# Performance work log

Hardware: AMD Instinct MI355X
Metric: run time of the kernel (lower is better)

Reference implementation:

```python
import jax, jax.numpy as jnp
import numpy as np

TS = 6      # texture cube size (hard-coded in module)
S = 256     # image size (NMR default / ref image size)
DIST = 2.732


def _look_at(verts, eye):
    # NMR look_at: camera at eye, looking at origin, up=(0,1,0)
    eye = jnp.asarray(eye, verts.dtype)
    z = -eye / jnp.linalg.norm(eye)
    up = jnp.array([0.0, 1.0, 0.0], verts.dtype)
    x = jnp.cross(up, z)
    x = x / jnp.linalg.norm(x)
    y = jnp.cross(z, x)
    R = jnp.stack([x, y, z])          # rows = camera axes
    return (verts - eye) @ R.T


def _render(verts, faces, tex_flat, eye):
    # verts [V,3], faces [F,3] int, tex_flat [F*TS^3, 3] (tanh already applied)
    v = _look_at(verts, eye)
    fv = v[faces]                      # [F,3,3]
    p0, p1, p2 = fv[:, 0], fv[:, 1], fv[:, 2]
    ps = (2.0 * jnp.arange(S, dtype=verts.dtype) + 1.0 - S) / S
    PX = jnp.broadcast_to(ps[None, :], (S, S)).reshape(-1)      # x right
    PY = jnp.broadcast_to(-ps[:, None], (S, S)).reshape(-1)     # y up (row 0 = top)

    def edge(a, b):
        # signed edge function, [F,HW]
        return ((PX[None, :] - a[:, 0:1]) * (b[:, 1:2] - a[:, 1:2])
                - (PY[None, :] - a[:, 1:2]) * (b[:, 0:1] - a[:, 0:1]))

    e0 = edge(p1, p2)
    e1 = edge(p2, p0)
    e2 = edge(p0, p1)
    # per-face signed area (double area) [F,1]
    area = ((p1[:, 0] - p0[:, 0]) * (p2[:, 1] - p0[:, 1])
            - (p1[:, 1] - p0[:, 1]) * (p2[:, 0] - p0[:, 0]))[:, None]
    ok = jnp.abs(area) > 1e-8
    inv = jnp.where(ok, 1.0 / jnp.where(ok, area, 1.0), 0.0)
    w0, w1, w2 = e0 * inv, e1 * inv, e2 * inv            # barycentric weights
    inside = (w0 >= 0) & (w1 >= 0) & (w2 >= 0) & ok       # both windings (fill_back)
    z = w0 * p0[:, 2:3] + w1 * p1[:, 2:3] + w2 * p2[:, 2:3]
    depth = jnp.where(inside & (z > 0), z, jnp.inf)       # z-buffer candidates
    best = jnp.argmin(depth, axis=0)                      # [HW] winning face
    hit = jnp.take_along_axis(depth, best[None, :], axis=0)[0] < jnp.inf
    wb = jnp.stack([jnp.take_along_axis(w, best[None, :], axis=0)[0]
                    for w in (w0, w1, w2)], axis=-1)       # [HW,3]
    ti = jnp.clip(jnp.round(wb * (TS - 1)), 0, TS - 1).astype(jnp.int32)
    flat = ((best * TS + ti[:, 0]) * TS + ti[:, 1]) * TS + ti[:, 2]
    colors = tex_flat[flat]                                # [HW,3] gather
    img = jnp.where(hit[:, None], colors, 0.0)
    return img.reshape(S, S, 3).transpose(2, 0, 1)[None]   # [1,3,S,S]


def setup_inputs() -> dict:
    key = jax.random.key(0)
    k1, k2, k3, k4, k5 = jax.random.split(key, 5)
    V, F = 252, 500
    return {
        "vertices": jax.random.normal(k1, (1, V, 3), jnp.float32),
        "faces": jax.random.randint(k2, (1, F, 3), 0, V, jnp.int64),
        "textures": jax.random.normal(k3, (1, F, TS, TS, TS, 3), jnp.float32),
        "image_ref": jax.random.uniform(k4, (1, 3, S, S), jnp.float32),
        "image_ref_2": jax.random.uniform(k5, (1, 3, S, S), jnp.float32),
    }


def reference(vertices, faces, textures, image_ref, image_ref_2):
    tex_flat = jnp.tanh(textures[0]).reshape(-1, 3)
    v, f = vertices[0], faces[0]
    # eye = get_points_from_angles(2.732, 180, 0) -> (0, 0, +d)
    img1 = _render(v, f, tex_flat, jnp.array([0.0, 0.0, DIST], jnp.float32))
    loss_one_side = jnp.sum((img1 - image_ref) ** 2)
    # eye = get_points_from_angles(2.732, 0, 0) -> (0, 0, -d)
    img2 = _render(v, f, tex_flat, jnp.array([0.0, 0.0, -DIST], jnp.float32))
    loss_symmetric = jnp.sum((img2 - image_ref_2) ** 2)
    return (loss_one_side + loss_symmetric) / 2
```

## Files before the change

kernel.cpp:

```cpp
#include <hip/hip_runtime.h>
#include <math.h>

#define IMG_S 256
#define NPIX (IMG_S * IMG_S)
#define NFACE 500
#define NCHUNK 16
#define FPC 32
#define PPT 8
#define TSZ 6
#define DIST 2.732f

struct FaceCoef {
    float A0, B0, C0, A1, B1, C1, A2, B2, C2, Az, Bz, Cz;
};

__device__ __forceinline__ void edge_coef(float ax, float ay, float bx, float by,
                                          float inv, float& A, float& B, float& C) {
    float dy = by - ay;
    float dx = bx - ax;
    A = dy * inv;
    B = -dx * inv;
    C = (ay * dx - ax * dy) * inv;
}

__device__ __forceinline__ FaceCoef compute_face(const float* __restrict__ verts,
                                                 const int* __restrict__ faces,
                                                 int f, int view) {
    int i0 = faces[f * 3 + 0];
    int i1 = faces[f * 3 + 1];
    int i2 = faces[f * 3 + 2];

    float v0x = verts[i0 * 3 + 0], v0y = verts[i0 * 3 + 1], v0z = verts[i0 * 3 + 2];
    float v1x = verts[i1 * 3 + 0], v1y = verts[i1 * 3 + 1], v1z = verts[i1 * 3 + 2];
    float v2x = verts[i2 * 3 + 0], v2y = verts[i2 * 3 + 1], v2z = verts[i2 * 3 + 2];

    float p0x, p0y, p0z, p1x, p1y, p1z, p2x, p2y, p2z;
    if (view == 0) {
        p0x = -v0x; p0y = v0y; p0z = DIST - v0z;
        p1x = -v1x; p1y = v1y; p1z = DIST - v1z;
        p2x = -v2x; p2y = v2y; p2z = DIST - v2z;
    } else {
        p0x = v0x; p0y = v0y; p0z = v0z + DIST;
        p1x = v1x; p1y = v1y; p1z = v1z + DIST;
        p2x = v2x; p2y = v2y; p2z = v2z + DIST;
    }

    float area = (p1x - p0x) * (p2y - p0y) - (p1y - p0y) * (p2x - p0x);
    bool ok = fabsf(area) > 1e-8f;

    FaceCoef fc;
    if (ok) {
        float inv = 1.0f / area;
        edge_coef(p1x, p1y, p2x, p2y, inv, fc.A0, fc.B0, fc.C0);
        edge_coef(p2x, p2y, p0x, p0y, inv, fc.A1, fc.B1, fc.C1);
        edge_coef(p0x, p0y, p1x, p1y, inv, fc.A2, fc.B2, fc.C2);
        fc.Az = fc.A0 * p0z + fc.A1 * p1z + fc.A2 * p2z;
        fc.Bz = fc.B0 * p0z + fc.B1 * p1z + fc.B2 * p2z;
        fc.Cz = fc.C0 * p0z + fc.C1 * p1z + fc.C2 * p2z;
    } else {
        fc.A0 = fc.B0 = fc.A1 = fc.B1 = fc.A2 = fc.B2 = 0.0f;
        fc.C0 = fc.C1 = fc.C2 = -1.0f;
        fc.Az = fc.Bz = fc.Cz = 0.0f;
    }
    return fc;
}

__device__ __forceinline__ float pix_x(int ix) {
    return (2.0f * (float)ix + 1.0f - (float)IMG_S) * (1.0f / (float)IMG_S);
}
__device__ __forceinline__ float pix_y(int iy) {
    return -((2.0f * (float)iy + 1.0f - (float)IMG_S) * (1.0f / (float)IMG_S));
}

__global__ __launch_bounds__(256) void raster_chunk_kernel(
    const float* __restrict__ verts,
    const int*   __restrict__ faces,
    unsigned long long* __restrict__ packed_out)
{
    __shared__ float4 fc[FPC][3];
    const int tile  = blockIdx.x;
    const int chunk = blockIdx.y;
    const int view  = blockIdx.z;
    const int fbase = chunk * FPC;

    if ((int)threadIdx.x < FPC) {
        int f = fbase + (int)threadIdx.x;
        FaceCoef c;
        if (f < NFACE) {
            c = compute_face(verts, faces, f, view);
        } else {
            c.A0 = c.B0 = c.A1 = c.B1 = c.A2 = c.B2 = 0.0f;
            c.C0 = c.C1 = c.C2 = -1.0f;
            c.Az = c.Bz = c.Cz = 0.0f;
        }
        fc[threadIdx.x][0] = make_float4(c.A0, c.B0, c.C0, c.A1);
        fc[threadIdx.x][1] = make_float4(c.B1, c.C1, c.A2, c.B2);
        fc[threadIdx.x][2] = make_float4(c.C2, c.Az, c.Bz, c.Cz);
    }
    __syncthreads();

    const int ix = threadIdx.x;
    const float px = pix_x(ix);
    float py[PPT];
    #pragma unroll
    for (int k = 0; k < PPT; ++k) py[k] = pix_y(tile * PPT + k);

    float bestz[PPT];
    int   besti[PPT];
    #pragma unroll
    for (int k = 0; k < PPT; ++k) { bestz[k] = INFINITY; besti[k] = -1; }

    float4 n0 = fc[0][0], n1 = fc[0][1], n2 = fc[0][2];
    #pragma unroll 4
    for (int f = 0; f < FPC; ++f) {
        float4 q0 = n0, q1 = n1, q2 = n2;
        int fn = (f + 1) & (FPC - 1);
        n0 = fc[fn][0]; n1 = fc[fn][1]; n2 = fc[fn][2];

        float d0 = fmaf(px, q0.x, q0.z);
        float d1 = fmaf(px, q0.w, q1.y);
        float d2 = fmaf(px, q1.z, q2.x);
        float dz = fmaf(px, q2.y, q2.w);
        #pragma unroll
        for (int k = 0; k < PPT; ++k) {
            float w0 = fmaf(q0.y, py[k], d0);
            float w1 = fmaf(q1.x, py[k], d1);
            float w2 = fmaf(q1.w, py[k], d2);
            float z  = fmaf(q2.z, py[k], dz);
            float wmin = fminf(w0, fminf(w1, w2));
            float s = fminf(z, bestz[k] - z);
            bool cc = (wmin >= 0.0f) && (s > 0.0f);
            bestz[k] = cc ? z : bestz[k];
            besti[k] = cc ? f : besti[k];
        }
    }

    unsigned long long* __restrict__ outp =
        packed_out + (size_t)(view * NCHUNK + chunk) * NPIX + tile * (PPT * IMG_S) + ix;
    #pragma unroll
    for (int k = 0; k < PPT; ++k) {
        unsigned long long packed;
        if (besti[k] >= 0)
            packed = ((unsigned long long)__float_as_uint(bestz[k]) << 32) |
                     (unsigned int)(fbase + besti[k]);
        else
            packed = ~0ull;
        outp[k * IMG_S] = packed;
    }
}

__global__ __launch_bounds__(256) void shade_loss_kernel(
    const float* __restrict__ verts,
    const int*   __restrict__ faces,
    const float* __restrict__ tex,
    const float* __restrict__ ref0,
    const float* __restrict__ ref1,
    const unsigned long long* __restrict__ packed_in,
    float* __restrict__ partials)
{
    __shared__ float red[4];
    const int gid  = blockIdx.x * blockDim.x + threadIdx.x;
    const int view = gid >> 16;
    const int pix  = gid & (NPIX - 1);

    const unsigned long long* p = packed_in + (size_t)view * NCHUNK * NPIX + pix;
    unsigned long long best = p[0];
    #pragma unroll
    for (int c = 1; c < NCHUNK; ++c) {
        unsigned long long v = p[(size_t)c * NPIX];
        best = (v < best) ? v : best;
    }

    float c0 = 0.0f, c1 = 0.0f, c2 = 0.0f;
    if (best != ~0ull) {
        int fidx = (int)(best & 0xFFFFFFFFu);
        FaceCoef fcw = compute_face(verts, faces, fidx, view);
        const float px = pix_x(pix & (IMG_S - 1));
        const float py = pix_y(pix >> 8);
        float w0 = fmaf(fcw.B0, py, fmaf(px, fcw.A0, fcw.C0));
        float w1 = fmaf(fcw.B1, py, fmaf(px, fcw.A1, fcw.C1));
        float w2 = fmaf(fcw.B2, py, fmaf(px, fcw.A2, fcw.C2));
        int t0 = (int)fminf(fmaxf(rintf(w0 * (float)(TSZ - 1)), 0.0f), (float)(TSZ - 1));
        int t1 = (int)fminf(fmaxf(rintf(w1 * (float)(TSZ - 1)), 0.0f), (float)(TSZ - 1));
        int t2 = (int)fminf(fmaxf(rintf(w2 * (float)(TSZ - 1)), 0.0f), (float)(TSZ - 1));
        int flat = ((fidx * TSZ + t0) * TSZ + t1) * TSZ + t2;
        const float* t = tex + (long)flat * 3;
        c0 = tanhf(t[0]);
        c1 = tanhf(t[1]);
        c2 = tanhf(t[2]);
    }

    const float* __restrict__ ref = (view == 0) ? ref0 : ref1;
    float d0 = c0 - ref[0 * NPIX + pix];
    float d1 = c1 - ref[1 * NPIX + pix];
    float d2 = c2 - ref[2 * NPIX + pix];
    float acc = fmaf(d0, d0, fmaf(d1, d1, d2 * d2));

    for (int off = 32; off > 0; off >>= 1)
        acc += __shfl_down(acc, off, 64);
    int lane = threadIdx.x & 63;
    int wid = threadIdx.x >> 6;
    if (lane == 0) red[wid] = acc;
    __syncthreads();
    if (threadIdx.x == 0)
        partials[blockIdx.x] = red[0] + red[1] + red[2] + red[3];
}

__global__ __launch_bounds__(256) void reduce_kernel(const float* __restrict__ partials,
                                                     int n, float* __restrict__ out) {
    __shared__ float red[4];
    float v = 0.0f;
    for (int i = threadIdx.x; i < n; i += 256) v += partials[i];
    for (int off = 32; off > 0; off >>= 1)
        v += __shfl_down(v, off, 64);
    int lane = threadIdx.x & 63;
    int wid = threadIdx.x >> 6;
    if (lane == 0) red[wid] = v;
    __syncthreads();
    if (threadIdx.x == 0)
        out[0] = 0.5f * (red[0] + red[1] + red[2] + red[3]);
}

extern "C" void kernel_launch(void* const* d_in, const int* in_sizes, int n_in,
                              void* d_out, int out_size, void* d_ws, size_t ws_size,
                              hipStream_t stream) {
    const float* verts = (const float*)d_in[0];
    const int*   faces = (const int*)d_in[1];
    const float* tex   = (const float*)d_in[2];
    const float* ref0  = (const float*)d_in[3];
    const float* ref1  = (const float*)d_in[4];
    float* out = (float*)d_out;

    unsigned long long* packed = (unsigned long long*)d_ws;
    float* partials = (float*)((char*)d_ws + (size_t)2 * NCHUNK * NPIX * 8);

    dim3 grid1(NPIX / (256 * PPT), NCHUNK, 2);
    raster_chunk_kernel<<<grid1, 256, 0, stream>>>(verts, faces, packed);

    const int shade_blocks = (2 * NPIX) / 256;
    shade_loss_kernel<<<shade_blocks, 256, 0, stream>>>(verts, faces, tex, ref0, ref1,
                                                        packed, partials);
    reduce_kernel<<<1, 256, 0, stream>>>(partials, shade_blocks, out);
}
```

Before: 90.76 us.

## Cull faces per row tile and merge chunk z-buffers with atomicMin

Each raster block now drops faces whose y-extent misses its 8-row tile, or that lie entirely behind the camera, and compacts the survivors with a ballot. The inner loop then iterates only over visible faces. Per-chunk results are merged straight into a single z-buffer per view with 64-bit atomicMin, so the shade kernel reads one value instead of 16 and the separate reduce kernel becomes a float atomicAdd. This cuts the 16x packed buffer traffic and the wasted edge tests. It adds two memsets, atomic contention and a non-deterministic float summation order.

```diff
diff --git a/kernel.cpp b/kernel.cpp
--- a/kernel.cpp
+++ b/kernel.cpp
@@ -23,9 +23,10 @@
     C = (ay * dx - ax * dy) * inv;
 }
 
-__device__ __forceinline__ FaceCoef compute_face(const float* __restrict__ verts,
-                                                 const int* __restrict__ faces,
-                                                 int f, int view) {
+__device__ __forceinline__ bool compute_face_bbox(const float* __restrict__ verts,
+                                                  const int* __restrict__ faces,
+                                                  int f, int view, FaceCoef& fc,
+                                                  float& ymin, float& ymax, float& zmax) {
     int i0 = faces[f * 3 + 0];
     int i1 = faces[f * 3 + 1];
     int i2 = faces[f * 3 + 2];
@@ -45,24 +46,22 @@
         p2x = v2x; p2y = v2y; p2z = v2z + DIST;
     }
 
+    ymin = fminf(p0y, fminf(p1y, p2y));
+    ymax = fmaxf(p0y, fmaxf(p1y, p2y));
+    zmax = fmaxf(p0z, fmaxf(p1z, p2z));
+
     float area = (p1x - p0x) * (p2y - p0y) - (p1y - p0y) * (p2x - p0x);
     bool ok = fabsf(area) > 1e-8f;
-
-    FaceCoef fc;
-    if (ok) {
-        float inv = 1.0f / area;
-        edge_coef(p1x, p1y, p2x, p2y, inv, fc.A0, fc.B0, fc.C0);
-        edge_coef(p2x, p2y, p0x, p0y, inv, fc.A1, fc.B1, fc.C1);
-        edge_coef(p0x, p0y, p1x, p1y, inv, fc.A2, fc.B2, fc.C2);
-        fc.Az = fc.A0 * p0z + fc.A1 * p1z + fc.A2 * p2z;
-        fc.Bz = fc.B0 * p0z + fc.B1 * p1z + fc.B2 * p2z;
-        fc.Cz = fc.C0 * p0z + fc.C1 * p1z + fc.C2 * p2z;
-    } else {
-        fc.A0 = fc.B0 = fc.A1 = fc.B1 = fc.A2 = fc.B2 = 0.0f;
-        fc.C0 = fc.C1 = fc.C2 = -1.0f;
-        fc.Az = fc.Bz = fc.Cz = 0.0f;
-    }
-    return fc;
+    if (!ok) return false;
+
+    float inv = 1.0f / area;
+    edge_coef(p1x, p1y, p2x, p2y, inv, fc.A0, fc.B0, fc.C0);
+    edge_coef(p2x, p2y, p0x, p0y, inv, fc.A1, fc.B1, fc.C1);
+    edge_coef(p0x, p0y, p1x, p1y, inv, fc.A2, fc.B2, fc.C2);
+    fc.Az = fc.A0 * p0z + fc.A1 * p1z + fc.A2 * p2z;
+    fc.Bz = fc.B0 * p0z + fc.B1 * p1z + fc.B2 * p2z;
+    fc.Cz = fc.C0 * p0z + fc.C1 * p1z + fc.C2 * p2z;
+    return true;
 }
 
 __device__ __forceinline__ float pix_x(int ix) {
@@ -75,29 +74,41 @@
 __global__ __launch_bounds__(256) void raster_chunk_kernel(
     const float* __restrict__ verts,
     const int*   __restrict__ faces,
-    unsigned long long* __restrict__ packed_out)
+    unsigned long long* __restrict__ zbuf)
 {
-    __shared__ float4 fc[FPC][3];
+    __shared__ float4 sc[FPC][3];
+    __shared__ int    sidx[FPC];
+    __shared__ int    scount;
+
     const int tile  = blockIdx.x;
     const int chunk = blockIdx.y;
     const int view  = blockIdx.z;
     const int fbase = chunk * FPC;
 
-    if ((int)threadIdx.x < FPC) {
-        int f = fbase + (int)threadIdx.x;
+    const float py_top = pix_y(tile * PPT);
+    const float py_bot = pix_y(tile * PPT + PPT - 1);
+
+    if (threadIdx.x < 64) {
+        bool keep = false;
         FaceCoef c;
-        if (f < NFACE) {
-            c = compute_face(verts, faces, f, view);
-        } else {
-            c.A0 = c.B0 = c.A1 = c.B1 = c.A2 = c.B2 = 0.0f;
-            c.C0 = c.C1 = c.C2 = -1.0f;
-            c.Az = c.Bz = c.Cz = 0.0f;
-        }
-        fc[threadIdx.x][0] = make_float4(c.A0, c.B0, c.C0, c.A1);
-        fc[threadIdx.x][1] = make_float4(c.B1, c.C1, c.A2, c.B2);
-        fc[threadIdx.x][2] = make_float4(c.C2, c.Az, c.Bz, c.Cz);
+        int fi = fbase + (int)threadIdx.x;
+        if ((int)threadIdx.x < FPC && fi < NFACE) {
+            float ymin, ymax, zmax;
+            bool ok = compute_face_bbox(verts, faces, fi, view, c, ymin, ymax, zmax);
+            keep = ok && (ymax >= py_bot) && (ymin <= py_top) && (zmax > 0.0f);
+        }
+        unsigned long long bal = __ballot(keep);
+        int pos = __popcll(bal & ((1ull << (threadIdx.x & 63)) - 1ull));
+        if (keep) {
+            sc[pos][0] = make_float4(c.A0, c.B0, c.C0, c.A1);
+            sc[pos][1] = make_float4(c.B1, c.C1, c.A2, c.B2);
+            sc[pos][2] = make_float4(c.C2, c.Az, c.Bz, c.Cz);
+            sidx[pos] = fi;
+        }
+        if (threadIdx.x == 0) scount = (int)__popcll(bal);
     }
     __syncthreads();
+    const int cnt = scount;
 
     const int ix = threadIdx.x;
     const float px = pix_x(ix);
@@ -106,17 +117,14 @@
     for (int k = 0; k < PPT; ++k) py[k] = pix_y(tile * PPT + k);
 
     float bestz[PPT];
-    int   besti[PPT];
+    int   bestj[PPT];
     #pragma unroll
-    for (int k = 0; k < PPT; ++k) { bestz[k] = INFINITY; besti[k] = -1; }
-
-    float4 n0 = fc[0][0], n1 = fc[0][1], n2 = fc[0][2];
-    #pragma unroll 4
-    for (int f = 0; f < FPC; ++f) {
-        float4 q0 = n0, q1 = n1, q2 = n2;
-        int fn = (f + 1) & (FPC - 1);
-        n0 = fc[fn][0]; n1 = fc[fn][1]; n2 = fc[fn][2];
-
+    for (int k = 0; k < PPT; ++k) { bestz[k] = INFINITY; bestj[k] = -1; }
+
+    for (int j = 0; j < cnt; ++j) {
+        float4 q0 = sc[j][0];
+        float4 q1 = sc[j][1];
+        float4 q2 = sc[j][2];
         float d0 = fmaf(px, q0.x, q0.z);
         float d1 = fmaf(px, q0.w, q1.y);
         float d2 = fmaf(px, q1.z, q2.x);
@@ -131,21 +139,19 @@
             float s = fminf(z, bestz[k] - z);
             bool cc = (wmin >= 0.0f) && (s > 0.0f);
             bestz[k] = cc ? z : bestz[k];
-            besti[k] = cc ? f : besti[k];
-        }
-    }
-
-    unsigned long long* __restrict__ outp =
-        packed_out + (size_t)(view * NCHUNK + chunk) * NPIX + tile * (PPT * IMG_S) + ix;
+            bestj[k] = cc ? j : bestj[k];
+        }
+    }
+
+    unsigned long long* __restrict__ zb = zbuf + (size_t)view * NPIX;
     #pragma unroll
     for (int k = 0; k < PPT; ++k) {
-        unsigned long long packed;
-        if (besti[k] >= 0)
-            packed = ((unsigned long long)__float_as_uint(bestz[k]) << 32) |
-                     (unsigned int)(fbase + besti[k]);
-        else
-            packed = ~0ull;
-        outp[k * IMG_S] = packed;
+        if (bestj[k] >= 0) {
+            unsigned long long packed =
+                ((unsigned long long)__float_as_uint(bestz[k]) << 32) |
+                (unsigned int)sidx[bestj[k]];
+            atomicMin(&zb[(tile * PPT + k) * IMG_S + ix], packed);
+        }
     }
 }
 
@@ -155,26 +161,22 @@
     const float* __restrict__ tex,
     const float* __restrict__ ref0,
     const float* __restrict__ ref1,
-    const unsigned long long* __restrict__ packed_in,
-    float* __restrict__ partials)
+    const unsigned long long* __restrict__ zbuf,
+    float* __restrict__ out)
 {
     __shared__ float red[4];
     const int gid  = blockIdx.x * blockDim.x + threadIdx.x;
     const int view = gid >> 16;
     const int pix  = gid & (NPIX - 1);
 
-    const unsigned long long* p = packed_in + (size_t)view * NCHUNK * NPIX + pix;
-    unsigned long long best = p[0];
-    #pragma unroll
-    for (int c = 1; c < NCHUNK; ++c) {
-        unsigned long long v = p[(size_t)c * NPIX];
-        best = (v < best) ? v : best;
-    }
+    unsigned long long best = zbuf[(size_t)view * NPIX + pix];
 
     float c0 = 0.0f, c1 = 0.0f, c2 = 0.0f;
     if (best != ~0ull) {
         int fidx = (int)(best & 0xFFFFFFFFu);
-        FaceCoef fcw = compute_face(verts, faces, fidx, view);
+        FaceCoef fcw;
+        float ymin, ymax, zmax;
+        compute_face_bbox(verts, faces, fidx, view, fcw, ymin, ymax, zmax);
         const float px = pix_x(pix & (IMG_S - 1));
         const float py = pix_y(pix >> 8);
         float w0 = fmaf(fcw.B0, py, fmaf(px, fcw.A0, fcw.C0));
@@ -203,22 +205,7 @@
     if (lane == 0) red[wid] = acc;
     __syncthreads();
     if (threadIdx.x == 0)
-        partials[blockIdx.x] = red[0] + red[1] + red[2] + red[3];
-}
-
-__global__ __launch_bounds__(256) void reduce_kernel(const float* __restrict__ partials,
-                                                     int n, float* __restrict__ out) {
-    __shared__ float red[4];
-    float v = 0.0f;
-    for (int i = threadIdx.x; i < n; i += 256) v += partials[i];
-    for (int off = 32; off > 0; off >>= 1)
-        v += __shfl_down(v, off, 64);
-    int lane = threadIdx.x & 63;
-    int wid = threadIdx.x >> 6;
-    if (lane == 0) red[wid] = v;
-    __syncthreads();
-    if (threadIdx.x == 0)
-        out[0] = 0.5f * (red[0] + red[1] + red[2] + red[3]);
+        atomicAdd(out, 0.5f * (red[0] + red[1] + red[2] + red[3]));
 }
 
 extern "C" void kernel_launch(void* const* d_in, const int* in_sizes, int n_in,
@@ -231,14 +218,15 @@
     const float* ref1  = (const float*)d_in[4];
     float* out = (float*)d_out;
 
-    unsigned long long* packed = (unsigned long long*)d_ws;
-    float* partials = (float*)((char*)d_ws + (size_t)2 * NCHUNK * NPIX * 8);
+    unsigned long long* zbuf = (unsigned long long*)d_ws;
+
+    hipMemsetAsync(zbuf, 0xFF, (size_t)2 * NPIX * sizeof(unsigned long long), stream);
+    hipMemsetAsync(out, 0, sizeof(float), stream);
 
     dim3 grid1(NPIX / (256 * PPT), NCHUNK, 2);
-    raster_chunk_kernel<<<grid1, 256, 0, stream>>>(verts, faces, packed);
+    raster_chunk_kernel<<<grid1, 256, 0, stream>>>(verts, faces, zbuf);
 
     const int shade_blocks = (2 * NPIX) / 256;
     shade_loss_kernel<<<shade_blocks, 256, 0, stream>>>(verts, faces, tex, ref0, ref1,
-                                                        packed, partials);
-    reduce_kernel<<<1, 256, 0, stream>>>(partials, shade_blocks, out);
-}
+                                                        zbuf, out);
+}
```

Measured after the change: 87.95 us. 1.03x faster.
